# Performance work log

Measured on AMD Instinct MI355X. Metric: run time of the kernel, lower is better.

Reference implementation:

```python
import jax, jax.numpy as jnp
import numpy as np

B, C, H, W = 8, 512, 96, 96
C8 = C // 8


def conv1x1(x, w, b):
    # x: (B,Cin,H,W), w: (Cout,Cin), b: (Cout,)
    return jnp.einsum('bchw,oc->bohw', x, w) + b[None, :, None, None]


def setup_inputs() -> dict:
    key = jax.random.key(0)
    ks = jax.random.split(key, 12)
    s = 0.05
    return {
        'x_exmplar': jax.random.normal(ks[0], (B, C, H, W), jnp.float32),
        'x_query': jax.random.normal(ks[1], (B, C, H, W), jnp.float32),
        'Wq': jax.random.normal(ks[2], (C8, C), jnp.float32) * s,
        'bq': jax.random.normal(ks[3], (C8,), jnp.float32) * s,
        'Wk': jax.random.normal(ks[4], (C8, C), jnp.float32) * s,
        'bk': jax.random.normal(ks[5], (C8,), jnp.float32) * s,
        'Wv': jax.random.normal(ks[6], (C, C), jnp.float32) * s,
        'bv': jax.random.normal(ks[7], (C,), jnp.float32) * s,
        'Wqv': jax.random.normal(ks[8], (C, C), jnp.float32) * s,
        'bqv': jax.random.normal(ks[9], (C,), jnp.float32) * s,
        'gamma1': jax.random.normal(ks[10], (1,), jnp.float32) * 0.5,
        'gamma2': jax.random.normal(ks[11], (1,), jnp.float32) * 0.5,
    }


def reference(x_exmplar, x_query, Wq, bq, Wk, bk, Wv, bv, Wqv, bqv, gamma1, gamma2):
    Bq, Cq, Hh, Ww = x_query.shape
    q = conv1x1(x_query, Wq, bq)        # (B,C8,H,W)
    k = conv1x1(x_exmplar, Wk, bk)      # (B,C8,H,W)
    v = conv1x1(x_exmplar, Wv, bv)      # (B,C,H,W)
    qv = conv1x1(x_query, Wqv, bqv)     # (B,C,H,W)

    # Criss-cross energies. energy_H masks the self position (INF diag).
    eH = jnp.einsum('bchw,bcjw->bhwj', q, k)            # (B,H,W,H)
    eye = jnp.eye(Hh, dtype=bool)                        # (H,H)
    eH = jnp.where(eye[:, None, :], -jnp.inf, eH)        # mask h==j
    eW = jnp.einsum('bchw,bchj->bhwj', q, k)             # (B,H,W,W)

    att = jax.nn.softmax(jnp.concatenate([eH, eW], axis=3), axis=3)
    att_H, att_W = att[..., :Hh], att[..., Hh:]          # (B,H,W,H),(B,H,W,W)

    out_H = jnp.einsum('bcjw,bhwj->bchw', v, att_H)
    out_W = jnp.einsum('bchj,bhwj->bchw', v, att_W)
    qout_H = jnp.einsum('bcjw,bhwj->bchw', qv, att_H)
    qout_W = jnp.einsum('bchj,bhwj->bchw', qv, att_W)

    # Diagonal (LR/RL) terms. Note: torch.diagonal of the transposed map equals
    # the diagonal itself, so energy_RL == energy_LR (faithful to original).
    qd = jnp.diagonal(q, axis1=2, axis2=3)               # (B,C8,D)
    kd = jnp.diagonal(k, axis1=2, axis2=3)
    vd = jnp.diagonal(v, axis1=2, axis2=3)               # (B,C,D)
    qvd = jnp.diagonal(qv, axis1=2, axis2=3)
    e_LR = jnp.einsum('bci,bcj->bij', kd, qd)            # (B,D,D)

    # softmax over a size-1 trailing axis (as in the original): yields ones,
    # broadcast-added over the width dim.
    out_LR = jax.nn.softmax(jnp.einsum('bcd,bdj->bcj', vd, e_LR)[..., None], axis=3)
    out_RL = jax.nn.softmax(jnp.einsum('bcd,bdj->bcj', vd, e_LR)[..., None], axis=3)
    qout_LR = jax.nn.softmax(jnp.einsum('bcd,bdj->bcj', qvd, e_LR)[..., None], axis=3)
    qout_RL = jax.nn.softmax(jnp.einsum('bcd,bdj->bcj', qvd, e_LR)[..., None], axis=3)

    examplar_att = out_H + out_W + out_LR + out_RL       # (B,C,H,W) via broadcast
    query_att = qout_H + qout_W + qout_LR + qout_RL
    return (gamma1 * examplar_att + x_exmplar, gamma2 * query_att + x_query)
```

## Files before the change

### kernel.cpp

```cpp
#include <hip/hip_runtime.h>
#include <math.h>

#define C_   512
#define C8_  64
#define HH   96
#define WW   96
#define PP   9216
#define CP   4718592
#define C8P  589824
#define ATTN 1769472

typedef __attribute__((ext_vector_type(4))) float f32x4;
typedef __attribute__((ext_vector_type(8))) __bf16 bf16x8;
typedef __attribute__((ext_vector_type(8))) unsigned short ushort8;
typedef __attribute__((ext_vector_type(4))) unsigned short ushort4v;
typedef __attribute__((ext_vector_type(2))) unsigned short ushort2v;
typedef __attribute__((ext_vector_type(2))) float float2v;

__device__ __forceinline__ float bf2f(unsigned short u) {
    union { unsigned u; float f; } x; x.u = ((unsigned)u) << 16; return x.f;
}
__device__ __forceinline__ unsigned short f2bf(float f) {
    union { float f; unsigned u; } x; x.f = f;
    unsigned r = x.u + 0x7fffu + ((x.u >> 16) & 1u);
    return (unsigned short)(r >> 16);
}
__device__ __forceinline__ void gload16(const void* g, void* l) {
    __builtin_amdgcn_global_load_lds(
        (const __attribute__((address_space(1))) unsigned int*)g,
        (__attribute__((address_space(3))) unsigned int*)l, 16, 0, 0);
}

__global__ __launch_bounds__(256) void cast_w(
    const float* __restrict__ Wv, const float* __restrict__ Wqv,
    const float* __restrict__ Wq, const float* __restrict__ Wk,
    unsigned short* __restrict__ oV, unsigned short* __restrict__ oQV,
    unsigned short* __restrict__ oQ, unsigned short* __restrict__ oK)
{
    int y = blockIdx.y;
    int n = (y < 2) ? 262144 : 32768;
    const float* s = (y == 0) ? Wv : (y == 1) ? Wqv : (y == 2) ? Wq : Wk;
    unsigned short* d = (y == 0) ? oV : (y == 1) ? oQV : (y == 2) ? oQ : oK;
    int i = (blockIdx.x * 256 + threadIdx.x) * 4;
    if (i < n) {
        float4 v = *(const float4*)(s + i);
        ushort4v o = { f2bf(v.x), f2bf(v.y), f2bf(v.z), f2bf(v.w) };
        *(ushort4v*)(d + i) = o;
    }
}

__global__ __launch_bounds__(256) void cast_transpose_cp(
    const float* __restrict__ xq, const float* __restrict__ xe,
    unsigned short* __restrict__ xTq, unsigned short* __restrict__ xTe)
{
    int zz = blockIdx.z;
    int which = zz & 1;
    size_t b = zz >> 1;
    const float* xb = (which ? xe : xq) + b * (size_t)CP;
    unsigned short* xTb = (which ? xTe : xTq) + b * (size_t)CP;
    int p0 = blockIdx.x * 64, c0 = blockIdx.y * 64;

    __shared__ unsigned short T[64][65];
    int t = threadIdx.x;
    int pp = t & 31, cg = t >> 5;
#pragma unroll
    for (int i = 0; i < 8; ++i) {
        int c = cg + 8 * i;
        float2v v = *(const float2v*)(xb + (size_t)(c0 + c) * PP + p0 + pp * 2);
        T[c][pp * 2] = f2bf(v.x);
        T[c][pp * 2 + 1] = f2bf(v.y);
    }
    __syncthreads();
    int cp = t & 31;
#pragma unroll
    for (int i = 0; i < 8; ++i) {
        int e = t + 256 * i;
        int p = e >> 5;
        ushort2v o = { T[cp * 2][p], T[cp * 2 + 1][p] };
        *(ushort2v*)(xTb + (size_t)(p0 + p) * C_ + c0 + cp * 2) = o;
    }
}

__global__ __launch_bounds__(256) void gemm_qk(
    const unsigned short* __restrict__ Wqb, const unsigned short* __restrict__ Wkb,
    const unsigned short* __restrict__ xTq, const unsigned short* __restrict__ xTe,
    const float* __restrict__ bq, const float* __restrict__ bk,
    unsigned short* __restrict__ qout, unsigned short* __restrict__ kout)
{
    int sel = blockIdx.y;
    const unsigned short* A = sel ? Wkb : Wqb;
    const float* bias = sel ? bk : bq;
    int p0 = blockIdx.x * 128;
    size_t b = blockIdx.z;
    const unsigned short* Bb = (sel ? xTe : xTq) + b * (size_t)CP;
    unsigned short* outb = (sel ? kout : qout) + b * (size_t)C8P;

    __shared__ __align__(16) unsigned short Asm[2][64 * 32];
    __shared__ __align__(16) unsigned short Bsm[2][128 * 32];

    int tid = threadIdx.x;
    int lane = tid & 63, wid = tid >> 6;
    int wr = wid >> 1, wc = wid & 1;
    int l15 = lane & 15, l4 = lane >> 4;
    f32x4 acc[2][4] = {};

#define QK_STAGE(KT, BUF)                                                              \
    {                                                                                  \
        int k0s = (KT) * 32;                                                           \
        int c = tid;                                                                   \
        gload16(A + (size_t)(c >> 2) * 512 + k0s + (c & 3) * 8, Asm[BUF] + c * 8);     \
        gload16(Bb + (size_t)(p0 + (c >> 2)) * 512 + k0s + (c & 3) * 8, Bsm[BUF] + c * 8); \
        int cb = tid + 256;                                                            \
        gload16(Bb + (size_t)(p0 + (cb >> 2)) * 512 + k0s + (cb & 3) * 8, Bsm[BUF] + cb * 8); \
    }

    QK_STAGE(0, 0);
    QK_STAGE(1, 1);

#pragma unroll
    for (int k = 0; k < 16; ++k) {
        int cur = k & 1;
        if (k < 15) asm volatile("s_waitcnt vmcnt(3)" ::: "memory");
        else        asm volatile("s_waitcnt vmcnt(0)" ::: "memory");
        __builtin_amdgcn_s_barrier();
        bf16x8 af[2], bfr[4];
#pragma unroll
        for (int m = 0; m < 2; ++m)
            af[m] = *(const bf16x8*)&Asm[cur][(wr * 32 + m * 16 + l15) * 32 + l4 * 8];
#pragma unroll
        for (int n = 0; n < 4; ++n)
            bfr[n] = *(const bf16x8*)&Bsm[cur][(wc * 64 + n * 16 + l15) * 32 + l4 * 8];
#pragma unroll
        for (int m = 0; m < 2; ++m)
#pragma unroll
            for (int n = 0; n < 4; ++n)
                acc[m][n] = __builtin_amdgcn_mfma_f32_16x16x32_bf16(af[m], bfr[n], acc[m][n], 0, 0, 0);
        asm volatile("" ::: "memory");
        __builtin_amdgcn_s_barrier();
        if (k < 14) QK_STAGE(k + 2, cur);
    }
#undef QK_STAGE

#pragma unroll
    for (int m = 0; m < 2; ++m)
#pragma unroll
        for (int n = 0; n < 4; ++n) {
            int pcol = p0 + wc * 64 + n * 16 + l15;
#pragma unroll
            for (int r = 0; r < 4; ++r) {
                int orow = wr * 32 + m * 16 + l4 * 4 + r;
                outb[(size_t)orow * PP + pcol] = f2bf(acc[m][n][r] + bias[orow]);
            }
        }
}

__global__ __launch_bounds__(256) void thw_b(
    const unsigned short* __restrict__ in, unsigned short* __restrict__ out)
{
    size_t m = blockIdx.x;
    const unsigned short* im = in + m * (size_t)PP;
    unsigned short* om = out + m * (size_t)PP;
    __shared__ unsigned short T[96][97];
    int t = threadIdx.x;
#pragma unroll
    for (int i = 0; i < 18; ++i) {
        int v = t + 256 * i;
        int r = v / 48, pp = v - r * 48;
        ushort2v u = *(const ushort2v*)(im + r * 96 + pp * 2);
        T[r][pp * 2] = u.x;
        T[r][pp * 2 + 1] = u.y;
    }
    __syncthreads();
#pragma unroll
    for (int i = 0; i < 18; ++i) {
        int v = t + 256 * i;
        int w = v / 48, hh = v - w * 48;
        ushort2v o = { T[hh * 2][w], T[hh * 2 + 1][w] };
        *(ushort2v*)(om + w * 96 + hh * 2) = o;
    }
}

__global__ __launch_bounds__(256) void scores_kernel(
    const unsigned short* __restrict__ qT, const unsigned short* __restrict__ kT,
    const unsigned short* __restrict__ q, const unsigned short* __restrict__ k,
    unsigned short* __restrict__ attb, float* __restrict__ rsum0, float* __restrict__ rsum1)
{
    int s = blockIdx.x;
    int ori = blockIdx.y;
    size_t b = blockIdx.z;
    const unsigned short* qs = (ori ? q : qT) + b * (size_t)C8P;
    const unsigned short* ks = (ori ? k : kT) + b * (size_t)C8P;
    unsigned short* ab = attb + b * (size_t)ATTN;
    float* rs = (ori ? rsum1 : rsum0) + b * (size_t)PP;

    __shared__ float Qs[64][97];
    __shared__ float Ks[64][97];
    int t = threadIdx.x;
    for (int v = t; v < 64 * 12; v += 256) {
        int c = v / 12, gg = v - c * 12;
        size_t gi = (size_t)c * PP + (size_t)s * 96 + gg * 8;
        ushort8 uq = *(const ushort8*)(qs + gi);
        ushort8 uk = *(const ushort8*)(ks + gi);
#pragma unroll
        for (int kk = 0; kk < 8; ++kk) {
            Qs[c][gg * 8 + kk] = bf2f(uq[kk]);
            Ks[c][gg * 8 + kk] = bf2f(uk[kk]);
        }
    }
    __syncthreads();
    int tx = t & 15, ty = t >> 4;
    float acc[6][6] = {};
    for (int c = 0; c < 64; ++c) {
        float qf[6], kf[6];
#pragma unroll
        for (int i = 0; i < 6; ++i) { qf[i] = Qs[c][ty + 16 * i]; kf[i] = Ks[c][tx + 16 * i]; }
#pragma unroll
        for (int i = 0; i < 6; ++i)
#pragma unroll
            for (int j = 0; j < 6; ++j) acc[i][j] = fmaf(qf[i], kf[j], acc[i][j]);
    }
#pragma unroll
    for (int i = 0; i < 6; ++i) {
        int m = ty + 16 * i;
        size_t row = ori ? ((size_t)s * 96 + m) : ((size_t)m * 96 + s);
        unsigned short* rowp = ab + row * 192 + (ori ? 96 : 0);
        float part = 0.0f;
#pragma unroll
        for (int j = 0; j < 6; ++j) {
            int jj = tx + 16 * j;
            float e = (!ori && jj == m) ? 0.0f : __expf(acc[i][j] - 20.0f);
            part += e;
            rowp[jj] = f2bf(e);
        }
#pragma unroll
        for (int off = 1; off < 16; off <<= 1) part += __shfl_xor(part, off);
        if (tx == 0) rs[row] = part;
    }
}

template<int ORI>
__global__ __launch_bounds__(512) void apply_mfma(
    const unsigned short* __restrict__ xT_e, const unsigned short* __restrict__ xT_q,
    unsigned short* __restrict__ yT_e, unsigned short* __restrict__ yT_q,
    const unsigned short* __restrict__ attb,
    const float* __restrict__ rsum0, const float* __restrict__ rsum1)
{
    int s = blockIdx.x;
    int path = blockIdx.y >> 1, ct = blockIdx.y & 1;
    int c0 = ct * 256;
    size_t b = blockIdx.z;
    const unsigned short* X = (path ? xT_q : xT_e) + b * (size_t)CP;
    unsigned short* Y = (path ? yT_q : yT_e) + b * (size_t)CP;
    const unsigned short* ab = attb + b * (size_t)ATTN;
    const float* r0 = rsum0 + b * (size_t)PP;
    const float* r1 = rsum1 + b * (size_t)PP;

    __shared__ __align__(16) unsigned short Att[96][104];
    __shared__ __align__(16) unsigned short Xs[256][104];

    int tid = threadIdx.x;
    for (int v = tid; v < 96 * 12; v += 512) {
        int r = v / 12, gg = v - r * 12;
        size_t base = ORI ? ((size_t)(s * 96 + r) * 192 + 96) : ((size_t)(r * 96 + s) * 192);
        *(ushort8*)&Att[r][gg * 8] = *(const ushort8*)(ab + base + gg * 8);
    }
    for (int v = tid; v < 96 * 32; v += 512) {
        int j = v >> 5, cc = v & 31;
        size_t pj = ORI ? ((size_t)s * 96 + j) : ((size_t)j * 96 + s);
        ushort8 u = *(const ushort8*)(X + pj * C_ + c0 + cc * 8);
        int js = j ^ ((cc & 3) << 3);
#pragma unroll
        for (int e = 0; e < 8; ++e) Xs[cc * 8 + e][js] = u[e];
    }
    __syncthreads();

    int lane = tid & 63, wid = tid >> 6;
    int wm = wid >> 2, wn = wid & 3;
    int l15 = lane & 15, l4 = lane >> 4;
    f32x4 acc[3][4] = {};
#pragma unroll
    for (int k = 0; k < 3; ++k) {
        bf16x8 a[3], xx[4];
#pragma unroll
        for (int mi = 0; mi < 3; ++mi)
            a[mi] = *(const bf16x8*)&Att[wm * 48 + mi * 16 + l15][k * 32 + l4 * 8];
#pragma unroll
        for (int ni = 0; ni < 4; ++ni) {
            int row = wn * 64 + ni * 16 + l15;
            int gsw = (k * 4 + l4) ^ ((row >> 3) & 3);
            xx[ni] = *(const bf16x8*)&Xs[row][gsw * 8];
        }
#pragma unroll
        for (int mi = 0; mi < 3; ++mi)
#pragma unroll
            for (int ni = 0; ni < 4; ++ni)
                acc[mi][ni] = __builtin_amdgcn_mfma_f32_16x16x32_bf16(a[mi], xx[ni], acc[mi][ni], 0, 0, 0);
    }

#pragma unroll
    for (int mi = 0; mi < 3; ++mi) {
#pragma unroll
        for (int r = 0; r < 4; ++r) {
            int mrow = wm * 48 + mi * 16 + l4 * 4 + r;
            size_t p = ORI ? ((size_t)s * 96 + mrow) : ((size_t)mrow * 96 + s);
            float rinv = 0.0f;
            if (ORI) rinv = 1.0f / (r0[p] + r1[p]);
            size_t base = p * C_ + c0;
#pragma unroll
            for (int ni = 0; ni < 4; ++ni) {
                size_t idx = base + wn * 64 + ni * 16 + l15;
                if (ORI == 0) {
                    Y[idx] = f2bf(acc[mi][ni][r]);
                } else {
                    float tot = bf2f(Y[idx]) + acc[mi][ni][r];
                    Y[idx] = f2bf(tot * rinv);
                }
            }
        }
    }
}

__global__ __launch_bounds__(512) void gemm_out(
    const unsigned short* __restrict__ Wvb, const unsigned short* __restrict__ Wqvb,
    const unsigned short* __restrict__ yT_e, const unsigned short* __restrict__ yT_q,
    const float* __restrict__ bv, const float* __restrict__ bqv,
    const float* __restrict__ xe, const float* __restrict__ xq,
    const float* __restrict__ g1, const float* __restrict__ g2,
    float* __restrict__ o0, float* __restrict__ o1)
{
    int yy = blockIdx.y;
    int path = yy >> 2, ot = yy & 3;
    const unsigned short* A = path ? Wqvb : Wvb;
    const float* bias = path ? bqv : bv;
    int p0 = blockIdx.x * 128;
    int o0r = ot * 128;
    size_t b = blockIdx.z;
    const unsigned short* Bb = (path ? yT_q : yT_e) + b * (size_t)CP;
    const float* xb = (path ? xq : xe) + b * (size_t)CP;
    float* ob = (path ? o1 : o0) + b * (size_t)CP;
    float gam = (path ? g2 : g1)[0];

    __shared__ __align__(16) unsigned short Asm[2][128 * 64];
    __shared__ __align__(16) unsigned short Bsm[2][128 * 64];

    int tid = threadIdx.x;
    int lane = tid & 63, wid = tid >> 6;
    int wr = wid >> 2, wc = wid & 3;
    int l15 = lane & 15, l4 = lane >> 4;
    f32x4 acc[4][2] = {};

#define GO_STAGE(KT, BUF)                                                                  \
    {                                                                                      \
        int k0s = (KT) * 64;                                                               \
        _Pragma("unroll")                                                                  \
        for (int i = 0; i < 2; ++i) {                                                      \
            int ch = tid + i * 512;                                                        \
            int row = ch >> 3, slot = ch & 7;                                              \
            int gs = slot ^ (row & 7);                                                     \
            gload16(A + (size_t)(o0r + row) * 512 + k0s + gs * 8, Asm[BUF] + ch * 8);      \
            gload16(Bb + (size_t)(p0 + row) * 512 + k0s + gs * 8, Bsm[BUF] + ch * 8);      \
        }                                                                                  \
    }

    GO_STAGE(0, 0);
    GO_STAGE(1, 1);

#pragma unroll
    for (int k = 0; k < 8; ++k) {
        int cur = k & 1;
        if (k < 7) asm volatile("s_waitcnt vmcnt(4)" ::: "memory");
        else       asm volatile("s_waitcnt vmcnt(0)" ::: "memory");
        __builtin_amdgcn_s_barrier();
#pragma unroll
        for (int ks = 0; ks < 2; ++ks) {
            bf16x8 af[4], bfr[2];
#pragma unroll
            for (int m = 0; m < 4; ++m) {
                int row = wr * 64 + m * 16 + l15;
                int sl = (ks * 4 + l4) ^ (row & 7);
                af[m] = *(const bf16x8*)&Asm[cur][row * 64 + sl * 8];
            }
#pragma unroll
            for (int n = 0; n < 2; ++n) {
                int row = wc * 32 + n * 16 + l15;
                int sl = (ks * 4 + l4) ^ (row & 7);
                bfr[n] = *(const bf16x8*)&Bsm[cur][row * 64 + sl * 8];
            }
#pragma unroll
            for (int m = 0; m < 4; ++m)
#pragma unroll
                for (int n = 0; n < 2; ++n)
                    acc[m][n] = __builtin_amdgcn_mfma_f32_16x16x32_bf16(af[m], bfr[n], acc[m][n], 0, 0, 0);
        }
        asm volatile("" ::: "memory");
        __builtin_amdgcn_s_barrier();
        if (k < 6) GO_STAGE(k + 2, cur);
    }
#undef GO_STAGE

#pragma unroll
    for (int m = 0; m < 4; ++m)
#pragma unroll
        for (int n = 0; n < 2; ++n) {
            int pcol = p0 + wc * 32 + n * 16 + l15;
#pragma unroll
            for (int r = 0; r < 4; ++r) {
                int orow = o0r + wr * 64 + m * 16 + l4 * 4 + r;
                size_t idx = (size_t)orow * PP + pcol;
                float val = acc[m][n][r] + bias[orow];
                ob[idx] = gam * (val + 2.0f) + xb[idx];
            }
        }
}

extern "C" void kernel_launch(void* const* d_in, const int* in_sizes, int n_in,
                              void* d_out, int out_size, void* d_ws, size_t ws_size,
                              hipStream_t stream)
{
    const float* x_ex = (const float*)d_in[0];
    const float* x_q  = (const float*)d_in[1];
    const float* Wq   = (const float*)d_in[2];
    const float* bq   = (const float*)d_in[3];
    const float* Wk   = (const float*)d_in[4];
    const float* bk   = (const float*)d_in[5];
    const float* Wv   = (const float*)d_in[6];
    const float* bv   = (const float*)d_in[7];
    const float* Wqv  = (const float*)d_in[8];
    const float* bqv  = (const float*)d_in[9];
    const float* g1   = (const float*)d_in[10];
    const float* g2   = (const float*)d_in[11];
    float* out0 = (float*)d_out;
    float* out1 = out0 + (size_t)8 * CP;

    unsigned short* hp = (unsigned short*)d_ws;
    unsigned short* Wvb  = hp; hp += 262144;
    unsigned short* Wqvb = hp; hp += 262144;
    unsigned short* Wqb  = hp; hp += 32768;
    unsigned short* Wkb  = hp; hp += 32768;
    size_t head = (size_t)(hp - (unsigned short*)d_ws) * 2;

    size_t perB = 4ull * CP + (size_t)ATTN + 4ull * C8P + 4ull * PP;
    int g = 8;
    while (g > 1 && head + (size_t)g * perB * 2 > ws_size) g >>= 1;

    unsigned short* p = hp;
    unsigned short* xT_e = p; p += (size_t)g * CP;
    unsigned short* xT_q = p; p += (size_t)g * CP;
    unsigned short* yT_e = p; p += (size_t)g * CP;
    unsigned short* yT_q = p; p += (size_t)g * CP;
    unsigned short* attb = p; p += (size_t)g * ATTN;
    unsigned short* qb   = p; p += (size_t)g * C8P;
    unsigned short* kb   = p; p += (size_t)g * C8P;
    unsigned short* qTb  = p; p += (size_t)g * C8P;
    unsigned short* kTb  = p; p += (size_t)g * C8P;
    float* rsum0 = (float*)p; p += (size_t)g * PP * 2;
    float* rsum1 = (float*)p; p += (size_t)g * PP * 2;

    cast_w<<<dim3(256, 4), 256, 0, stream>>>(Wv, Wqv, Wq, Wk, Wvb, Wqvb, Wqb, Wkb);

    for (int b0 = 0; b0 < 8; b0 += g) {
        const float* xe = x_ex + (size_t)b0 * CP;
        const float* xq = x_q  + (size_t)b0 * CP;
        float* o0 = out0 + (size_t)b0 * CP;
        float* o1 = out1 + (size_t)b0 * CP;

        cast_transpose_cp<<<dim3(144, 8, 2 * g), 256, 0, stream>>>(xq, xe, xT_q, xT_e);
        gemm_qk<<<dim3(72, 2, g), 256, 0, stream>>>(Wqb, Wkb, xT_q, xT_e, bq, bk, qb, kb);
        thw_b<<<dim3(2 * g * 64), 256, 0, stream>>>(qb, qTb);
        scores_kernel<<<dim3(96, 2, g), 256, 0, stream>>>(qTb, kTb, qb, kb, attb, rsum0, rsum1);
        apply_mfma<0><<<dim3(96, 4, g), 512, 0, stream>>>(xT_e, xT_q, yT_e, yT_q, attb, rsum0, rsum1);
        apply_mfma<1><<<dim3(96, 4, g), 512, 0, stream>>>(xT_e, xT_q, yT_e, yT_q, attb, rsum0, rsum1);
        gemm_out<<<dim3(72, 8, g), 512, 0, stream>>>(Wvb, Wqvb, yT_e, yT_q, bv, bqv,
                                                     xe, xq, g1, g2, o0, o1);
    }
}
```

Baseline: 573.9 us.

## Use 4-buffer LDS ring with 3-stage prefetch and swizzle in QK and output GEMMs

Both the Q/K projection GEMM and the final value/output GEMM move from double buffering to a four-slot LDS ring. Each prefetches three stages ahead, and the trailing barrier per iteration is removed. The output GEMM also shrinks its K-tile from 64 to 32, so it runs 16 iterations instead of 8. Both kernels apply an XOR swizzle keyed on (row>>1)&3 to cut LDS bank conflicts. The goal is to hide global-load latency and drop one barrier per step, at the cost of more in-flight loads and the loop overhead of smaller K steps.

```diff
diff --git a/kernel.cpp b/kernel.cpp
--- a/kernel.cpp
+++ b/kernel.cpp
@@ -95,8 +95,8 @@
     const unsigned short* Bb = (sel ? xTe : xTq) + b * (size_t)CP;
     unsigned short* outb = (sel ? kout : qout) + b * (size_t)C8P;
 
-    __shared__ __align__(16) unsigned short Asm[2][64 * 32];
-    __shared__ __align__(16) unsigned short Bsm[2][128 * 32];
+    __shared__ __align__(16) unsigned short Asm[4][64 * 32];
+    __shared__ __align__(16) unsigned short Bsm[4][128 * 32];
 
     int tid = threadIdx.x;
     int lane = tid & 63, wid = tid >> 6;
@@ -104,40 +104,52 @@
     int l15 = lane & 15, l4 = lane >> 4;
     f32x4 acc[2][4] = {};
 
-#define QK_STAGE(KT, BUF)                                                              \
-    {                                                                                  \
-        int k0s = (KT) * 32;                                                           \
-        int c = tid;                                                                   \
-        gload16(A + (size_t)(c >> 2) * 512 + k0s + (c & 3) * 8, Asm[BUF] + c * 8);     \
-        gload16(Bb + (size_t)(p0 + (c >> 2)) * 512 + k0s + (c & 3) * 8, Bsm[BUF] + c * 8); \
-        int cb = tid + 256;                                                            \
-        gload16(Bb + (size_t)(p0 + (cb >> 2)) * 512 + k0s + (cb & 3) * 8, Bsm[BUF] + cb * 8); \
+#define QK_STAGE(KT, BUF)                                                                   \
+    {                                                                                       \
+        int k0s = (KT) * 32;                                                                \
+        int ra = tid >> 2, sa = tid & 3;                                                    \
+        int ga = sa ^ ((ra >> 1) & 3);                                                      \
+        gload16(A + (size_t)ra * 512 + k0s + ga * 8, Asm[BUF] + tid * 8);                   \
+        _Pragma("unroll")                                                                   \
+        for (int i = 0; i < 2; ++i) {                                                       \
+            int ch = tid + i * 256;                                                         \
+            int rb = ch >> 2, sb = ch & 3;                                                  \
+            int gb = sb ^ ((rb >> 1) & 3);                                                  \
+            gload16(Bb + (size_t)(p0 + rb) * 512 + k0s + gb * 8, Bsm[BUF] + ch * 8);        \
+        }                                                                                   \
     }
 
     QK_STAGE(0, 0);
     QK_STAGE(1, 1);
+    QK_STAGE(2, 2);
 
 #pragma unroll
     for (int k = 0; k < 16; ++k) {
-        int cur = k & 1;
-        if (k < 15) asm volatile("s_waitcnt vmcnt(3)" ::: "memory");
-        else        asm volatile("s_waitcnt vmcnt(0)" ::: "memory");
+        int cur = k & 3;
+        if (k < 14)      asm volatile("s_waitcnt vmcnt(6)" ::: "memory");
+        else if (k < 15) asm volatile("s_waitcnt vmcnt(3)" ::: "memory");
+        else             asm volatile("s_waitcnt vmcnt(0)" ::: "memory");
         __builtin_amdgcn_s_barrier();
         bf16x8 af[2], bfr[4];
 #pragma unroll
-        for (int m = 0; m < 2; ++m)
-            af[m] = *(const bf16x8*)&Asm[cur][(wr * 32 + m * 16 + l15) * 32 + l4 * 8];
-#pragma unroll
-        for (int n = 0; n < 4; ++n)
-            bfr[n] = *(const bf16x8*)&Bsm[cur][(wc * 64 + n * 16 + l15) * 32 + l4 * 8];
+        for (int m = 0; m < 2; ++m) {
+            int row = wr * 32 + m * 16 + l15;
+            int sl = l4 ^ ((row >> 1) & 3);
+            af[m] = *(const bf16x8*)&Asm[cur][row * 32 + sl * 8];
+        }
+#pragma unroll
+        for (int n = 0; n < 4; ++n) {
+            int row = wc * 64 + n * 16 + l15;
+            int sl = l4 ^ ((row >> 1) & 3);
+            bfr[n] = *(const bf16x8*)&Bsm[cur][row * 32 + sl * 8];
+        }
 #pragma unroll
         for (int m = 0; m < 2; ++m)
 #pragma unroll
             for (int n = 0; n < 4; ++n)
                 acc[m][n] = __builtin_amdgcn_mfma_f32_16x16x32_bf16(af[m], bfr[n], acc[m][n], 0, 0, 0);
         asm volatile("" ::: "memory");
-        __builtin_amdgcn_s_barrier();
-        if (k < 14) QK_STAGE(k + 2, cur);
+        if (k < 13) QK_STAGE(k + 3, (k + 3) & 3);
     }
 #undef QK_STAGE
 
@@ -340,8 +352,8 @@
     float* ob = (path ? o1 : o0) + b * (size_t)CP;
     float gam = (path ? g2 : g1)[0];
 
-    __shared__ __align__(16) unsigned short Asm[2][128 * 64];
-    __shared__ __align__(16) unsigned short Bsm[2][128 * 64];
+    __shared__ __align__(16) unsigned short Asm[4][128 * 32];
+    __shared__ __align__(16) unsigned short Bsm[4][128 * 32];
 
     int tid = threadIdx.x;
     int lane = tid & 63, wid = tid >> 6;
@@ -349,52 +361,46 @@
     int l15 = lane & 15, l4 = lane >> 4;
     f32x4 acc[4][2] = {};
 
-#define GO_STAGE(KT, BUF)                                                                  \
-    {                                                                                      \
-        int k0s = (KT) * 64;                                                               \
-        _Pragma("unroll")                                                                  \
-        for (int i = 0; i < 2; ++i) {                                                      \
-            int ch = tid + i * 512;                                                        \
-            int row = ch >> 3, slot = ch & 7;                                              \
-            int gs = slot ^ (row & 7);                                                     \
-            gload16(A + (size_t)(o0r + row) * 512 + k0s + gs * 8, Asm[BUF] + ch * 8);      \
-            gload16(Bb + (size_t)(p0 + row) * 512 + k0s + gs * 8, Bsm[BUF] + ch * 8);      \
-        }                                                                                  \
+#define GO_STAGE(KT, BUF)                                                                   \
+    {                                                                                       \
+        int k0s = (KT) * 32;                                                                \
+        int row = tid >> 2, slot = tid & 3;                                                 \
+        int gs = slot ^ ((row >> 1) & 3);                                                   \
+        gload16(A + (size_t)(o0r + row) * 512 + k0s + gs * 8, Asm[BUF] + tid * 8);          \
+        gload16(Bb + (size_t)(p0 + row) * 512 + k0s + gs * 8, Bsm[BUF] + tid * 8);          \
     }
 
     GO_STAGE(0, 0);
     GO_STAGE(1, 1);
-
-#pragma unroll
-    for (int k = 0; k < 8; ++k) {
-        int cur = k & 1;
-        if (k < 7) asm volatile("s_waitcnt vmcnt(4)" ::: "memory");
-        else       asm volatile("s_waitcnt vmcnt(0)" ::: "memory");
+    GO_STAGE(2, 2);
+
+#pragma unroll
+    for (int k = 0; k < 16; ++k) {
+        int cur = k & 3;
+        if (k < 14)      asm volatile("s_waitcnt vmcnt(4)" ::: "memory");
+        else if (k < 15) asm volatile("s_waitcnt vmcnt(2)" ::: "memory");
+        else             asm volatile("s_waitcnt vmcnt(0)" ::: "memory");
         __builtin_amdgcn_s_barrier();
-#pragma unroll
-        for (int ks = 0; ks < 2; ++ks) {
-            bf16x8 af[4], bfr[2];
-#pragma unroll
-            for (int m = 0; m < 4; ++m) {
-                int row = wr * 64 + m * 16 + l15;
-                int sl = (ks * 4 + l4) ^ (row & 7);
-                af[m] = *(const bf16x8*)&Asm[cur][row * 64 + sl * 8];
-            }
-#pragma unroll
-            for (int n = 0; n < 2; ++n) {
-                int row = wc * 32 + n * 16 + l15;
-                int sl = (ks * 4 + l4) ^ (row & 7);
-                bfr[n] = *(const bf16x8*)&Bsm[cur][row * 64 + sl * 8];
-            }
-#pragma unroll
-            for (int m = 0; m < 4; ++m)
-#pragma unroll
-                for (int n = 0; n < 2; ++n)
-                    acc[m][n] = __builtin_amdgcn_mfma_f32_16x16x32_bf16(af[m], bfr[n], acc[m][n], 0, 0, 0);
-        }
+        bf16x8 af[4], bfr[2];
+#pragma unroll
+        for (int m = 0; m < 4; ++m) {
+            int row = wr * 64 + m * 16 + l15;
+            int sl = l4 ^ ((row >> 1) & 3);
+            af[m] = *(const bf16x8*)&Asm[cur][row * 32 + sl * 8];
+        }
+#pragma unroll
+        for (int n = 0; n < 2; ++n) {
+            int row = wc * 32 + n * 16 + l15;
+            int sl = l4 ^ ((row >> 1) & 3);
+            bfr[n] = *(const bf16x8*)&Bsm[cur][row * 32 + sl * 8];
+        }
+#pragma unroll
+        for (int m = 0; m < 4; ++m)
+#pragma unroll
+            for (int n = 0; n < 2; ++n)
+                acc[m][n] = __builtin_amdgcn_mfma_f32_16x16x32_bf16(af[m], bfr[n], acc[m][n], 0, 0, 0);
         asm volatile("" ::: "memory");
-        __builtin_amdgcn_s_barrier();
-        if (k < 6) GO_STAGE(k + 2, cur);
+        if (k < 13) GO_STAGE(k + 3, (k + 3) & 3);
     }
 #undef GO_STAGE
 
```

After: 591.1 us. 3.0% more time.
